# Performance work log

Hardware: AMD Instinct MI355X
Metric: run time of the kernel (lower is better)

## Reference

```python
import jax, jax.numpy as jnp
import numpy as np

K = 16          # buckets per codeblock (2**treeDepth)
DEPTH = 4       # tree depth
C = 256         # codeblockCount
IN_FEATURES = 4096
OUT_FEATURES = 4096
N_ROWS = 4096

_BASE_TREE = np.array([
    [-1,-1,0,-1,0,0,0,-1,0,0,0,0,0,0,0],[-1,-1,0,-1,0,0,0,1,0,0,0,0,0,0,0],
    [-1,-1,0,1,0,0,0,0,-1,0,0,0,0,0,0],[-1,-1,0,1,0,0,0,0,1,0,0,0,0,0,0],
    [-1,1,0,0,-1,0,0,0,0,-1,0,0,0,0,0],[-1,1,0,0,-1,0,0,0,0,1,0,0,0,0,0],
    [-1,1,0,0,1,0,0,0,0,0,-1,0,0,0,0],[-1,1,0,0,1,0,0,0,0,0,1,0,0,0,0],
    [1,0,-1,0,0,-1,0,0,0,0,0,-1,0,0,0],[1,0,-1,0,0,-1,0,0,0,0,0,1,0,0,0],
    [1,0,-1,0,0,1,0,0,0,0,0,0,-1,0,0],[1,0,-1,0,0,1,0,0,0,0,0,0,1,0,0],
    [1,0,1,0,0,0,-1,0,0,0,0,0,0,-1,0],[1,0,1,0,0,0,-1,0,0,0,0,0,0,1,0],
    [1,0,1,0,0,0,1,0,0,0,0,0,0,0,-1],[1,0,1,0,0,0,1,0,0,0,0,0,0,0,1]],
    dtype=np.float32)

def _make_tree_des_matrix(c):
    # NOTE: original code initializes with ONES, then overwrites diagonal blocks
    m = np.ones((c * K, c * (K - 1)), dtype=np.float32)
    for i in range(c):
        m[i*K:(i+1)*K, i*(K-1):(i+1)*(K-1)] = _BASE_TREE
    return m

def _make_selection_matrix(c):
    base = np.zeros((K - 1, DEPTH), dtype=np.float32)
    base[0, 0] = 1.0
    for i in range(1, K - 1):
        base[i, int(np.log2(i + 1))] = 1.0
    m = np.zeros((c * (K - 1), c * DEPTH), dtype=np.float32)
    for i in range(c):
        m[i*(K-1):(i+1)*(K-1), i*DEPTH:(i+1)*DEPTH] = base
    return m

def setup_inputs() -> dict:
    key = jax.random.key(0)
    k1, k2, k3, k4 = jax.random.split(key, 4)
    inputMatrix = jax.random.normal(k1, (N_ROWS, IN_FEATURES), dtype=jnp.float32)
    dims = jax.random.randint(k2, (C * DEPTH,), 0, IN_FEATURES)
    selection_matrix = jnp.asarray(_make_selection_matrix(C))
    thresholds = jax.random.normal(k3, (C * (K - 1), 1), dtype=jnp.float32)
    tree_des_mat = jnp.asarray(_make_tree_des_matrix(C))
    lut = jax.random.normal(k4, (OUT_FEATURES, C, K), dtype=jnp.float32)
    return {"inputMatrix": inputMatrix, "dims": dims,
            "selection_matrix": selection_matrix, "thresholds": thresholds,
            "tree_des_mat": tree_des_mat, "lut": lut}

def reference(inputMatrix, dims, selection_matrix, thresholds, tree_des_mat, lut):
    n = inputMatrix.shape[0]
    c = lut.shape[1]
    # gather the tree-split feature dims: (N, C*DEPTH)
    chosen = inputMatrix[:, dims]
    # (C*15, N)
    subtracted = selection_matrix @ chosen.T - thresholds
    tanh_h = jnp.tanh(subtracted)
    sign_ste = jnp.sign(subtracted) - jax.lax.stop_gradient(tanh_h) + tanh_h
    # (C*16, N) -> (N, C, 16)
    tree_result = (tree_des_mat @ sign_ste).T.reshape(n, c, K)
    encoding_soft = jax.nn.softmax(tree_result, axis=2)
    index = jnp.argmax(encoding_soft, axis=2)
    encoding_hard = jax.nn.one_hot(index, K, dtype=encoding_soft.dtype)
    Encoded = encoding_hard - jax.lax.stop_gradient(encoding_soft) + encoding_soft
    # LUT lookup: einsum 'nij,kij->nki' + sum over i, fused to 'nij,kij->nk'
    out = jnp.einsum('nij,kij->nk', Encoded, lut)
    return out
```

## Files before the change

### kernel.cpp

```cpp
#include <hip/hip_runtime.h>

#define N_ROWS 4096
#define IN_F   4096
#define OUT_F  4096
#define C_CB   256
#define KDIM   4096

typedef short bf16x8 __attribute__((ext_vector_type(8)));
typedef float f32x4  __attribute__((ext_vector_type(4)));

union ABFrag { unsigned long long u[2]; bf16x8 v; };

__device__ __forceinline__ unsigned int f2bf(float f) {
    unsigned int u = __builtin_bit_cast(unsigned int, f);
    return (u + 0x7FFFu + ((u >> 16) & 1u)) >> 16;
}

__global__ void k_idx(const float* __restrict__ input, const int* __restrict__ dims,
                      const float* __restrict__ thr, unsigned char* __restrict__ idx4) {
    const int n = blockIdx.x;
    const int c = threadIdx.x;
    const float* row = input + (size_t)n * IN_F;
    int4 d = *(const int4*)(dims + c * 4);
    const float* th = thr + c * 15;
    float x0 = row[d.x], x1 = row[d.y], x2 = row[d.z], x3 = row[d.w];
    int b0 = x0 > th[0];
    int j1 = 1 + b0;
    int b1 = x1 > th[j1];
    int j2 = 2 * j1 + 1 + b1;
    int b2 = x2 > th[j2];
    int j3 = 2 * j2 + 1 + b2;
    int b3 = x3 > th[j3];
    int idx = (b0 << 3) | (b1 << 2) | (b2 << 1) | b3;
    int other = __shfl_xor(idx, 1);
    if (!(c & 1))
        idx4[(c >> 1) * N_ROWS + n] = (unsigned char)(idx | (other << 4));
}

__global__ void k_cvt(const float* __restrict__ lut, unsigned short* __restrict__ lutb) {
    const int i = (blockIdx.x * blockDim.x + threadIdx.x) * 8;
    float4 a = *(const float4*)(lut + i);
    float4 b = *(const float4*)(lut + i + 4);
    uint4 o;
    o.x = f2bf(a.x) | (f2bf(a.y) << 16);
    o.y = f2bf(a.z) | (f2bf(a.w) << 16);
    o.z = f2bf(b.x) | (f2bf(b.y) << 16);
    o.w = f2bf(b.z) | (f2bf(b.w) << 16);
    *(uint4*)(lutb + i) = o;
}

#define BM 128
#define BN 128
#define BKT 64

template<bool STAGE_FP32>
__global__ __launch_bounds__(256, 4) void k_gemm(const unsigned short* __restrict__ lutb,
                                                 const float* __restrict__ lutf,
                                                 const unsigned char* __restrict__ idx4,
                                                 float* __restrict__ out) {
    __shared__ unsigned char smem[16384 + BN * BKT * 2];
    unsigned char* ish = smem;
    unsigned char* bsh = smem + 16384;

    const int t   = threadIdx.x;
    const int l15 = t & 15;
    const int q   = (t >> 4) & 3;
    const int w   = t >> 6;
    const int wm  = w >> 1, wn = w & 1;
    const int m0  = blockIdx.y * BM;
    const int n0  = blockIdx.x * BN;

    #pragma unroll
    for (int qq = 0; qq < 4; qq++) {
        int L = qq * 256 + t;
        const unsigned char* g = idx4 + (size_t)(L >> 3) * N_ROWS + m0 + (L & 7) * 16;
        __builtin_amdgcn_global_load_lds(
            (const __attribute__((address_space(1))) void*)g,
            (__attribute__((address_space(3))) void*)(ish + L * 16), 16, 0, 0);
    }

    f32x4 acc[4][4];
    #pragma unroll
    for (int mi = 0; mi < 4; mi++)
        #pragma unroll
        for (int ni = 0; ni < 4; ni++)
            acc[mi][ni] = (f32x4){0.f, 0.f, 0.f, 0.f};

    const int xorv = l15 & 7;
    const int bRowByte = (wn * 64 + l15) * (BKT * 2);
    const int aByte = wm * 64 + l15 * 4;
    const int qh4  = (q >> 1) * 4;
    const unsigned int sub8 = (q & 1) << 3;

    for (int kb = 0; kb < KDIM; kb += BKT) {
        if (!STAGE_FP32) {
            #pragma unroll
            for (int qq = 0; qq < 4; qq++) {
                int L = qq * 256 + t;
                int r = L >> 3, p = L & 7;
                int c = p ^ (r & 7);
                const unsigned short* g = lutb + (size_t)(n0 + r) * KDIM + kb + c * 8;
                __builtin_amdgcn_global_load_lds(
                    (const __attribute__((address_space(1))) void*)g,
                    (__attribute__((address_space(3))) void*)(bsh + L * 16), 16, 0, 0);
            }
        } else {
            #pragma unroll
            for (int qq = 0; qq < 4; qq++) {
                int L = qq * 256 + t;
                int r = L >> 3, p = L & 7;
                int c = p ^ (r & 7);
                const float* g = lutf + (size_t)(n0 + r) * KDIM + kb + c * 8;
                float4 f0 = *(const float4*)g;
                float4 f1 = *(const float4*)(g + 4);
                uint4 o;
                o.x = f2bf(f0.x) | (f2bf(f0.y) << 16);
                o.y = f2bf(f0.z) | (f2bf(f0.w) << 16);
                o.z = f2bf(f1.x) | (f2bf(f1.y) << 16);
                o.w = f2bf(f1.z) | (f2bf(f1.w) << 16);
                *(uint4*)(bsh + L * 16) = o;
            }
        }
        __syncthreads();

        #pragma unroll
        for (int s = 0; s < 2; s++) {
            const int cbp = (kb >> 5) + s;

            ABFrag bf[4];
            const int chunkOff = ((s * 4 + q) ^ xorv) * 16;
            #pragma unroll
            for (int ni = 0; ni < 4; ni++)
                bf[ni].v = *(const bf16x8*)(bsh + bRowByte + ni * (16 * BKT * 2) + chunkOff);

            const unsigned int w32 = *(const unsigned int*)(ish + cbp * 128 + aByte);

            ABFrag af[4];
            #pragma unroll
            for (int mi = 0; mi < 4; mi++) {
                unsigned int T = (w32 >> (mi * 8 + qh4)) & 0xFu;
                unsigned int rel = T - sub8;
                unsigned long long sh = 0x3F80ull << ((rel & 3) << 4);
                af[mi].u[0] = (rel < 4u) ? sh : 0ull;
                af[mi].u[1] = ((rel - 4u) < 4u) ? sh : 0ull;
            }

            #pragma unroll
            for (int mi = 0; mi < 4; mi++)
                #pragma unroll
                for (int ni = 0; ni < 4; ni++)
                    acc[mi][ni] = __builtin_amdgcn_mfma_f32_16x16x32_bf16(
                        af[mi].v, bf[ni].v, acc[mi][ni], 0, 0, 0);
        }
        __syncthreads();
    }

    #pragma unroll
    for (int mi = 0; mi < 4; mi++) {
        #pragma unroll
        for (int ni = 0; ni < 4; ni++) {
            const int col = n0 + wn * 64 + ni * 16 + l15;
            #pragma unroll
            for (int r = 0; r < 4; r++) {
                const int row = m0 + wm * 64 + 4 * (q * 4 + r) + mi;
                out[(size_t)row * OUT_F + col] = acc[mi][ni][r];
            }
        }
    }
}

extern "C" void kernel_launch(void* const* d_in, const int* in_sizes, int n_in,
                              void* d_out, int out_size, void* d_ws, size_t ws_size,
                              hipStream_t stream) {
    const float* input = (const float*)d_in[0];
    const int*   dims  = (const int*)d_in[1];
    const float* thr   = (const float*)d_in[3];
    const float* lut   = (const float*)d_in[5];
    float* out = (float*)d_out;

    const size_t lutbBytes = (size_t)OUT_F * KDIM * 2;
    const size_t idxBytes  = (size_t)(C_CB / 2) * N_ROWS;

    dim3 gg(OUT_F / BN, N_ROWS / BM);

    if (ws_size >= lutbBytes + idxBytes) {
        unsigned short* lutb = (unsigned short*)d_ws;
        unsigned char*  idx4 = (unsigned char*)d_ws + lutbBytes;
        k_idx<<<N_ROWS, C_CB, 0, stream>>>(input, dims, thr, idx4);
        k_cvt<<<(OUT_F * KDIM) / (256 * 8), 256, 0, stream>>>(lut, lutb);
        k_gemm<false><<<gg, 256, 0, stream>>>(lutb, lut, idx4, out);
    } else {
        unsigned char* idx4 = (unsigned char*)d_ws;
        k_idx<<<N_ROWS, C_CB, 0, stream>>>(input, dims, thr, idx4);
        k_gemm<true><<<gg, 256, 0, stream>>>(nullptr, lut, idx4, out);
    }
}
```

Before: 315.1 us.

## Double-buffer LUT tiles, widen GEMM N-tile, merge prep kernels

The GEMM now keeps two LDS stages for the bf16 LUT tile and issues the next tile's global-to-LDS loads before computing the current one, so load latency overlaps MFMA work. The N tile grows from 128 to 256, with 4x8 accumulators per wave and occupancy lowered to 2 blocks per SM, to improve reuse of the A fragments. The index and convert kernels are merged into one launch to save a launch. The costs are higher register pressure and LDS use per block, and fewer blocks in flight to hide latency.

```diff
diff --git a/kernel.cpp b/kernel.cpp
--- a/kernel.cpp
+++ b/kernel.cpp
@@ -16,51 +16,57 @@
     return (u + 0x7FFFu + ((u >> 16) & 1u)) >> 16;
 }
 
-__global__ void k_idx(const float* __restrict__ input, const int* __restrict__ dims,
-                      const float* __restrict__ thr, unsigned char* __restrict__ idx4) {
-    const int n = blockIdx.x;
-    const int c = threadIdx.x;
-    const float* row = input + (size_t)n * IN_F;
-    int4 d = *(const int4*)(dims + c * 4);
-    const float* th = thr + c * 15;
-    float x0 = row[d.x], x1 = row[d.y], x2 = row[d.z], x3 = row[d.w];
-    int b0 = x0 > th[0];
-    int j1 = 1 + b0;
-    int b1 = x1 > th[j1];
-    int j2 = 2 * j1 + 1 + b1;
-    int b2 = x2 > th[j2];
-    int j3 = 2 * j2 + 1 + b2;
-    int b3 = x3 > th[j3];
-    int idx = (b0 << 3) | (b1 << 2) | (b2 << 1) | b3;
-    int other = __shfl_xor(idx, 1);
-    if (!(c & 1))
-        idx4[(c >> 1) * N_ROWS + n] = (unsigned char)(idx | (other << 4));
-}
-
-__global__ void k_cvt(const float* __restrict__ lut, unsigned short* __restrict__ lutb) {
-    const int i = (blockIdx.x * blockDim.x + threadIdx.x) * 8;
-    float4 a = *(const float4*)(lut + i);
-    float4 b = *(const float4*)(lut + i + 4);
-    uint4 o;
-    o.x = f2bf(a.x) | (f2bf(a.y) << 16);
-    o.y = f2bf(a.z) | (f2bf(a.w) << 16);
-    o.z = f2bf(b.x) | (f2bf(b.y) << 16);
-    o.w = f2bf(b.z) | (f2bf(b.w) << 16);
-    *(uint4*)(lutb + i) = o;
+#define CVT_BLOCKS ((OUT_F * KDIM) / (256 * 8))
+
+__global__ void k_prep(const float* __restrict__ input, const int* __restrict__ dims,
+                       const float* __restrict__ thr, unsigned char* __restrict__ idx4,
+                       const float* __restrict__ lut, unsigned short* __restrict__ lutb) {
+    const int b = blockIdx.x;
+    if (b < N_ROWS) {
+        const int n = b;
+        const int c = threadIdx.x;
+        const float* row = input + (size_t)n * IN_F;
+        int4 d = *(const int4*)(dims + c * 4);
+        const float* th = thr + c * 15;
+        float x0 = row[d.x], x1 = row[d.y], x2 = row[d.z], x3 = row[d.w];
+        int b0 = x0 > th[0];
+        int j1 = 1 + b0;
+        int b1 = x1 > th[j1];
+        int j2 = 2 * j1 + 1 + b1;
+        int b2 = x2 > th[j2];
+        int j3 = 2 * j2 + 1 + b2;
+        int b3 = x3 > th[j3];
+        int idx = (b0 << 3) | (b1 << 2) | (b2 << 1) | b3;
+        int other = __shfl_xor(idx, 1);
+        if (!(c & 1))
+            idx4[(c >> 1) * N_ROWS + n] = (unsigned char)(idx | (other << 4));
+    } else {
+        const int i = ((b - N_ROWS) * 256 + threadIdx.x) * 8;
+        float4 a = *(const float4*)(lut + i);
+        float4 f = *(const float4*)(lut + i + 4);
+        uint4 o;
+        o.x = f2bf(a.x) | (f2bf(a.y) << 16);
+        o.y = f2bf(a.z) | (f2bf(a.w) << 16);
+        o.z = f2bf(f.x) | (f2bf(f.y) << 16);
+        o.w = f2bf(f.z) | (f2bf(f.w) << 16);
+        *(uint4*)(lutb + i) = o;
+    }
 }
 
 #define BM 128
-#define BN 128
+#define BN 256
 #define BKT 64
+#define BSTAGE (BN * BKT * 2)
 
 template<bool STAGE_FP32>
-__global__ __launch_bounds__(256, 4) void k_gemm(const unsigned short* __restrict__ lutb,
+__global__ __launch_bounds__(256, 2) void k_gemm(const unsigned short* __restrict__ lutb,
                                                  const float* __restrict__ lutf,
                                                  const unsigned char* __restrict__ idx4,
                                                  float* __restrict__ out) {
-    __shared__ unsigned char smem[16384 + BN * BKT * 2];
-    unsigned char* ish = smem;
-    unsigned char* bsh = smem + 16384;
+    __shared__ unsigned char smem[16384 + 2 * BSTAGE];
+    unsigned char* ish  = smem;
+    unsigned char* bsh0 = smem + 16384;
+    unsigned char* bsh1 = smem + 16384 + BSTAGE;
 
     const int t   = threadIdx.x;
     const int l15 = t & 15;
@@ -79,38 +85,25 @@
             (__attribute__((address_space(3))) void*)(ish + L * 16), 16, 0, 0);
     }
 
-    f32x4 acc[4][4];
-    #pragma unroll
-    for (int mi = 0; mi < 4; mi++)
-        #pragma unroll
-        for (int ni = 0; ni < 4; ni++)
-            acc[mi][ni] = (f32x4){0.f, 0.f, 0.f, 0.f};
-
-    const int xorv = l15 & 7;
-    const int bRowByte = (wn * 64 + l15) * (BKT * 2);
-    const int aByte = wm * 64 + l15 * 4;
-    const int qh4  = (q >> 1) * 4;
-    const unsigned int sub8 = (q & 1) << 3;
-
-    for (int kb = 0; kb < KDIM; kb += BKT) {
+    auto stageB = [&](unsigned char* dst, int kbn) {
         if (!STAGE_FP32) {
             #pragma unroll
-            for (int qq = 0; qq < 4; qq++) {
+            for (int qq = 0; qq < 8; qq++) {
                 int L = qq * 256 + t;
                 int r = L >> 3, p = L & 7;
                 int c = p ^ (r & 7);
-                const unsigned short* g = lutb + (size_t)(n0 + r) * KDIM + kb + c * 8;
+                const unsigned short* g = lutb + (size_t)(n0 + r) * KDIM + kbn + c * 8;
                 __builtin_amdgcn_global_load_lds(
                     (const __attribute__((address_space(1))) void*)g,
-                    (__attribute__((address_space(3))) void*)(bsh + L * 16), 16, 0, 0);
+                    (__attribute__((address_space(3))) void*)(dst + L * 16), 16, 0, 0);
             }
         } else {
             #pragma unroll
-            for (int qq = 0; qq < 4; qq++) {
+            for (int qq = 0; qq < 8; qq++) {
                 int L = qq * 256 + t;
                 int r = L >> 3, p = L & 7;
                 int c = p ^ (r & 7);
-                const float* g = lutf + (size_t)(n0 + r) * KDIM + kb + c * 8;
+                const float* g = lutf + (size_t)(n0 + r) * KDIM + kbn + c * 8;
                 float4 f0 = *(const float4*)g;
                 float4 f1 = *(const float4*)(g + 4);
                 uint4 o;
@@ -118,20 +111,34 @@
                 o.y = f2bf(f0.z) | (f2bf(f0.w) << 16);
                 o.z = f2bf(f1.x) | (f2bf(f1.y) << 16);
                 o.w = f2bf(f1.z) | (f2bf(f1.w) << 16);
-                *(uint4*)(bsh + L * 16) = o;
-            }
-        }
-        __syncthreads();
-
+                *(uint4*)(dst + L * 16) = o;
+            }
+        }
+    };
+
+    f32x4 acc[4][8];
+    #pragma unroll
+    for (int mi = 0; mi < 4; mi++)
+        #pragma unroll
+        for (int ni = 0; ni < 8; ni++)
+            acc[mi][ni] = (f32x4){0.f, 0.f, 0.f, 0.f};
+
+    const int xorv = l15 & 7;
+    const int bRowByte = (wn * 128 + l15) * (BKT * 2);
+    const int aByte = wm * 64 + l15 * 4;
+    const int qh4  = (q >> 1) * 4;
+    const unsigned int sub8 = (q & 1) << 3;
+
+    auto computeT = [&](const unsigned char* bsrc, int kb) {
         #pragma unroll
         for (int s = 0; s < 2; s++) {
             const int cbp = (kb >> 5) + s;
 
-            ABFrag bf[4];
+            ABFrag bf[8];
             const int chunkOff = ((s * 4 + q) ^ xorv) * 16;
             #pragma unroll
-            for (int ni = 0; ni < 4; ni++)
-                bf[ni].v = *(const bf16x8*)(bsh + bRowByte + ni * (16 * BKT * 2) + chunkOff);
+            for (int ni = 0; ni < 8; ni++)
+                bf[ni].v = *(const bf16x8*)(bsrc + bRowByte + ni * (16 * BKT * 2) + chunkOff);
 
             const unsigned int w32 = *(const unsigned int*)(ish + cbp * 128 + aByte);
 
@@ -148,18 +155,40 @@
             #pragma unroll
             for (int mi = 0; mi < 4; mi++)
                 #pragma unroll
-                for (int ni = 0; ni < 4; ni++)
+                for (int ni = 0; ni < 8; ni++)
                     acc[mi][ni] = __builtin_amdgcn_mfma_f32_16x16x32_bf16(
                         af[mi].v, bf[ni].v, acc[mi][ni], 0, 0, 0);
         }
-        __syncthreads();
+    };
+
+    stageB(bsh0, 0);
+    asm volatile("s_waitcnt vmcnt(0) lgkmcnt(0)" ::: "memory");
+    __builtin_amdgcn_s_barrier();
+    __builtin_amdgcn_sched_barrier(0);
+
+    for (int kb = 0; kb < KDIM; kb += 2 * BKT) {
+        stageB(bsh1, kb + BKT);
+        __builtin_amdgcn_sched_barrier(0);
+        computeT(bsh0, kb);
+        asm volatile("s_waitcnt vmcnt(0) lgkmcnt(0)" ::: "memory");
+        __builtin_amdgcn_s_barrier();
+        __builtin_amdgcn_sched_barrier(0);
+
+        if (kb + 2 * BKT < KDIM) {
+            stageB(bsh0, kb + 2 * BKT);
+            __builtin_amdgcn_sched_barrier(0);
+        }
+        computeT(bsh1, kb + BKT);
+        asm volatile("s_waitcnt vmcnt(0) lgkmcnt(0)" ::: "memory");
+        __builtin_amdgcn_s_barrier();
+        __builtin_amdgcn_sched_barrier(0);
     }
 
     #pragma unroll
     for (int mi = 0; mi < 4; mi++) {
         #pragma unroll
-        for (int ni = 0; ni < 4; ni++) {
-            const int col = n0 + wn * 64 + ni * 16 + l15;
+        for (int ni = 0; ni < 8; ni++) {
+            const int col = n0 + wn * 128 + ni * 16 + l15;
             #pragma unroll
             for (int r = 0; r < 4; r++) {
                 const int row = m0 + wm * 64 + 4 * (q * 4 + r) + mi;
@@ -186,12 +215,11 @@
     if (ws_size >= lutbBytes + idxBytes) {
         unsigned short* lutb = (unsigned short*)d_ws;
         unsigned char*  idx4 = (unsigned char*)d_ws + lutbBytes;
-        k_idx<<<N_ROWS, C_CB, 0, stream>>>(input, dims, thr, idx4);
-        k_cvt<<<(OUT_F * KDIM) / (256 * 8), 256, 0, stream>>>(lut, lutb);
+        k_prep<<<N_ROWS + CVT_BLOCKS, 256, 0, stream>>>(input, dims, thr, idx4, lut, lutb);
         k_gemm<false><<<gg, 256, 0, stream>>>(lutb, lut, idx4, out);
     } else {
         unsigned char* idx4 = (unsigned char*)d_ws;
-        k_idx<<<N_ROWS, C_CB, 0, stream>>>(input, dims, thr, idx4);
+        k_prep<<<N_ROWS, 256, 0, stream>>>(input, dims, thr, idx4, lut, nullptr);
         k_gemm<true><<<gg, 256, 0, stream>>>(nullptr, lut, idx4, out);
     }
 }
```

Result: slower. 350.8 us (+11.3%).
